# Performance work log

Hardware: AMD Instinct MI355X
Metric: run time of the kernel (lower is better)

## Reference

```python
import jax, jax.numpy as jnp
import numpy as np


def setup_inputs() -> dict:
    key = jax.random.key(0)
    k1, k2 = jax.random.split(key)
    B, H, S, D = 2, 16, 2048, 64
    scores = jax.random.normal(k1, (B, H, S, S), dtype=jnp.float32)
    v = jax.random.normal(k2, (B, H, S, D), dtype=jnp.float32)
    return {"scores": scores, "v": v}


def reference(scores, v):
    # softmax over last dim of [B,H,S,S], then contract with V [B,H,S,D]
    prob = jax.nn.softmax(scores, axis=-1)
    return jnp.einsum('bhqk,bhkd->bhqd', prob, v)
```

## Files before the change

### kernel.cpp

```cpp
#include <hip/hip_runtime.h>
#include <hip/hip_bf16.h>

#define NBH     32
#define SEQ     2048
#define DIM     64
#define QBLK    64
#define KBLK    64
#define NCHUNK  (SEQ / KBLK)
#define PSTRIDE 72

typedef __attribute__((ext_vector_type(4))) float f32x4;
typedef __attribute__((ext_vector_type(8))) short bf16x8;

__device__ __forceinline__ unsigned short bfbits(float f) {
    return __builtin_bit_cast(unsigned short, __float2bfloat16(f));
}

__global__ __launch_bounds__(256)
void vprep_kernel(const float* __restrict__ v, unsigned short* __restrict__ wsv)
{
    const int blk = blockIdx.x;
    const int bh  = blk >> 5, t = blk & 31;
    const float* vp = v + ((size_t)bh * SEQ + t * KBLK) * DIM;
    unsigned short* op = wsv + (size_t)blk * 4096;

    for (int fl = threadIdx.x; fl < 512; fl += 256) {
        const int ks = fl >> 8, dt = (fl >> 6) & 3, lane = fl & 63;
        const int g = lane >> 4, c = lane & 15;
        const float* sp = vp + (ks * 32 + g * 8) * DIM + dt * 16 + c;
        bf16x8 frag;
#pragma unroll
        for (int j = 0; j < 8; ++j)
            frag[j] = (short)bfbits(sp[j * DIM]);
        *reinterpret_cast<bf16x8*>(op + fl * 8) = frag;
    }
}

__global__ __launch_bounds__(256, 4)
void softmaxv_kernel(const float* __restrict__ scores,
                     const unsigned short* __restrict__ vfrags,
                     float* __restrict__ out)
{
    __shared__ unsigned short p_lds[2][QBLK * PSTRIDE];
    __shared__ float l_lds[QBLK];

    const int tid  = threadIdx.x;
    const int w    = tid >> 6;
    const int lane = tid & 63;
    const int g    = lane >> 4;
    const int c    = lane & 15;

    const int bid = blockIdx.x;
    const int bh  = bid >> 5;
    const int qb  = bid & 31;
    const int q0  = qb * QBLK;

    const float* sp = scores + ((size_t)bh * SEQ + q0 + w * 16 + g) * SEQ + c * 4;
    const unsigned short* vb = vfrags + (size_t)bh * 32 * 4096 + lane * 8;

    float lsum[4] = {0.f, 0.f, 0.f, 0.f};
    f32x4 acc[4];
#pragma unroll
    for (int dt = 0; dt < 4; ++dt) acc[dt] = (f32x4)0.0f;

#define LOADS(dst, t)                                                          \
    {                                                                          \
        _Pragma("unroll")                                                      \
        for (int i = 0; i < 4; ++i)                                            \
            dst[i] = *reinterpret_cast<const f32x4*>(                          \
                sp + (size_t)(i * 4) * SEQ + (t) * KBLK);                      \
    }

    auto proc = [&](const f32x4 (&sreg)[4], int t, unsigned short* pbuf) {
        const unsigned short* vp = vb + t * 4096;
        bf16x8 vf[2][4];
#pragma unroll
        for (int ks = 0; ks < 2; ++ks)
#pragma unroll
            for (int dt = 0; dt < 4; ++dt)
                vf[ks][dt] = *reinterpret_cast<const bf16x8*>(vp + (ks * 4 + dt) * 512);

#pragma unroll
        for (int i = 0; i < 4; ++i) {
            f32x4 s4 = sreg[i];
            float p0 = __expf(s4[0]);
            float p1 = __expf(s4[1]);
            float p2 = __expf(s4[2]);
            float p3 = __expf(s4[3]);
            lsum[i] += (p0 + p1) + (p2 + p3);
            unsigned lo = (unsigned)bfbits(p0) | ((unsigned)bfbits(p1) << 16);
            unsigned hi = (unsigned)bfbits(p2) | ((unsigned)bfbits(p3) << 16);
            const int row = w * 16 + i * 4 + g;
            *reinterpret_cast<uint2*>(&pbuf[row * PSTRIDE + c * 4]) = make_uint2(lo, hi);
        }

        __syncthreads();

#pragma unroll
        for (int ks = 0; ks < 2; ++ks) {
            const bf16x8 a = *reinterpret_cast<const bf16x8*>(
                &pbuf[(w * 16 + c) * PSTRIDE + ks * 32 + g * 8]);
#pragma unroll
            for (int dt = 0; dt < 4; ++dt)
                acc[dt] = __builtin_amdgcn_mfma_f32_16x16x32_bf16(
                    a, vf[ks][dt], acc[dt], 0, 0, 0);
        }
    };

    f32x4 sA[4], sB[4];
    LOADS(sA, 0)
    for (int tt = 0; tt < NCHUNK / 2; ++tt) {
        const int t0 = 2 * tt, t1 = 2 * tt + 1;
        LOADS(sB, t1)
        proc(sA, t0, p_lds[0]);
        if (t1 + 1 < NCHUNK) LOADS(sA, t1 + 1)
        proc(sB, t1, p_lds[1]);
    }
#undef LOADS

#pragma unroll
    for (int i = 0; i < 4; ++i) {
        float l = lsum[i];
        l += __shfl_xor(l, 1);
        l += __shfl_xor(l, 2);
        l += __shfl_xor(l, 4);
        l += __shfl_xor(l, 8);
        if (c == 0) l_lds[w * 16 + i * 4 + g] = l;
    }
    __syncthreads();

    float* op = out + ((size_t)bh * SEQ + q0 + w * 16) * DIM;
    float rl[4];
#pragma unroll
    for (int r = 0; r < 4; ++r)
        rl[r] = 1.0f / l_lds[w * 16 + g * 4 + r];
#pragma unroll
    for (int dt = 0; dt < 4; ++dt)
#pragma unroll
        for (int r = 0; r < 4; ++r)
            op[(g * 4 + r) * DIM + dt * 16 + c] = acc[dt][r] * rl[r];
}

extern "C" void kernel_launch(void* const* d_in, const int* in_sizes, int n_in,
                              void* d_out, int out_size, void* d_ws, size_t ws_size,
                              hipStream_t stream)
{
    const float* scores = (const float*)d_in[0];
    const float* v      = (const float*)d_in[1];
    float* out          = (float*)d_out;
    unsigned short* wsv = (unsigned short*)d_ws;

    vprep_kernel<<<dim3(NBH * NCHUNK), dim3(256), 0, stream>>>(v, wsv);
    softmaxv_kernel<<<dim3(NBH * (SEQ / QBLK)), dim3(256), 0, stream>>>(scores, wsv, out);
}
```

Before: 138.3 us.

## Load scores directly in MFMA A-fragment layout, dropping LDS staging and barriers

Each lane now reads its score row segments in the exact layout the bf16 MFMA A operand expects, so exponentials are packed into register fragments directly. This removes the LDS write/read round trip of the probability tile and the per-chunk __syncthreads. Row sums are reduced with cross-lane shuffles instead of LDS. The global load pattern changes from 16 lanes covering one contiguous 64-float row segment to each lane reading two 32-byte pieces of its own row, which may reduce coalescing on a memory-bound stream.

After: 150.3 us. 1.09x slower.

```diff
diff --git a/kernel.cpp b/kernel.cpp
--- a/kernel.cpp
+++ b/kernel.cpp
@@ -7,7 +7,6 @@
 #define QBLK    64
 #define KBLK    64
 #define NCHUNK  (SEQ / KBLK)
-#define PSTRIDE 72
 
 typedef __attribute__((ext_vector_type(4))) float f32x4;
 typedef __attribute__((ext_vector_type(8))) short bf16x8;
@@ -41,9 +40,6 @@
                      const unsigned short* __restrict__ vfrags,
                      float* __restrict__ out)
 {
-    __shared__ unsigned short p_lds[2][QBLK * PSTRIDE];
-    __shared__ float l_lds[QBLK];
-
     const int tid  = threadIdx.x;
     const int w    = tid >> 6;
     const int lane = tid & 63;
@@ -55,90 +51,88 @@
     const int qb  = bid & 31;
     const int q0  = qb * QBLK;
 
-    const float* sp = scores + ((size_t)bh * SEQ + q0 + w * 16 + g) * SEQ + c * 4;
-    const unsigned short* vb = vfrags + (size_t)bh * 32 * 4096 + lane * 8;
+    const float* sp = scores + ((size_t)bh * SEQ + q0 + w * 16 + c) * SEQ + g * 8;
+    const unsigned short* vb = vfrags + (size_t)bh * NCHUNK * 4096 + lane * 8;
 
-    float lsum[4] = {0.f, 0.f, 0.f, 0.f};
     f32x4 acc[4];
 #pragma unroll
     for (int dt = 0; dt < 4; ++dt) acc[dt] = (f32x4)0.0f;
+    float lsum[4] = {0.f, 0.f, 0.f, 0.f};
 
-#define LOADS(dst, t)                                                          \
+#define SLOADS(dst, t)                                                         \
     {                                                                          \
-        _Pragma("unroll")                                                      \
-        for (int i = 0; i < 4; ++i)                                            \
-            dst[i] = *reinterpret_cast<const f32x4*>(                          \
-                sp + (size_t)(i * 4) * SEQ + (t) * KBLK);                      \
+        dst[0] = *reinterpret_cast<const f32x4*>(sp + (t) * 64 + 0);           \
+        dst[1] = *reinterpret_cast<const f32x4*>(sp + (t) * 64 + 4);           \
+        dst[2] = *reinterpret_cast<const f32x4*>(sp + (t) * 64 + 32);          \
+        dst[3] = *reinterpret_cast<const f32x4*>(sp + (t) * 64 + 36);          \
     }
 
-    auto proc = [&](const f32x4 (&sreg)[4], int t, unsigned short* pbuf) {
-        const unsigned short* vp = vb + t * 4096;
-        bf16x8 vf[2][4];
+#define VLOAD(vf, t)                                                           \
+    {                                                                          \
+        const unsigned short* vp = vb + (t) * 4096;                            \
+        _Pragma("unroll")                                                      \
+        for (int ks = 0; ks < 2; ++ks)                                         \
+            _Pragma("unroll")                                                  \
+            for (int dt = 0; dt < 4; ++dt)                                     \
+                vf[ks][dt] = *reinterpret_cast<const bf16x8*>(                 \
+                    vp + (ks * 4 + dt) * 512);                                 \
+    }
+
+    auto compute = [&](const f32x4 (&sreg)[4], const bf16x8 (&vf)[2][4]) {
+        bf16x8 pfrag[2];
+#pragma unroll
+        for (int ks = 0; ks < 2; ++ks) {
+            const f32x4 a = sreg[ks * 2], b = sreg[ks * 2 + 1];
+            float e0 = __expf(a[0]), e1 = __expf(a[1]);
+            float e2 = __expf(a[2]), e3 = __expf(a[3]);
+            float e4 = __expf(b[0]), e5 = __expf(b[1]);
+            float e6 = __expf(b[2]), e7 = __expf(b[3]);
+            lsum[ks * 2]     += (e0 + e1) + (e2 + e3);
+            lsum[ks * 2 + 1] += (e4 + e5) + (e6 + e7);
+            bf16x8 p;
+            p[0] = (short)bfbits(e0); p[1] = (short)bfbits(e1);
+            p[2] = (short)bfbits(e2); p[3] = (short)bfbits(e3);
+            p[4] = (short)bfbits(e4); p[5] = (short)bfbits(e5);
+            p[6] = (short)bfbits(e6); p[7] = (short)bfbits(e7);
+            pfrag[ks] = p;
+        }
 #pragma unroll
         for (int ks = 0; ks < 2; ++ks)
 #pragma unroll
             for (int dt = 0; dt < 4; ++dt)
-                vf[ks][dt] = *reinterpret_cast<const bf16x8*>(vp + (ks * 4 + dt) * 512);
-
-#pragma unroll
-        for (int i = 0; i < 4; ++i) {
-            f32x4 s4 = sreg[i];
-            float p0 = __expf(s4[0]);
-            float p1 = __expf(s4[1]);
-            float p2 = __expf(s4[2]);
-            float p3 = __expf(s4[3]);
-            lsum[i] += (p0 + p1) + (p2 + p3);
-            unsigned lo = (unsigned)bfbits(p0) | ((unsigned)bfbits(p1) << 16);
-            unsigned hi = (unsigned)bfbits(p2) | ((unsigned)bfbits(p3) << 16);
-            const int row = w * 16 + i * 4 + g;
-            *reinterpret_cast<uint2*>(&pbuf[row * PSTRIDE + c * 4]) = make_uint2(lo, hi);
-        }
-
-        __syncthreads();
-
-#pragma unroll
-        for (int ks = 0; ks < 2; ++ks) {
-            const bf16x8 a = *reinterpret_cast<const bf16x8*>(
-                &pbuf[(w * 16 + c) * PSTRIDE + ks * 32 + g * 8]);
-#pragma unroll
-            for (int dt = 0; dt < 4; ++dt)
                 acc[dt] = __builtin_amdgcn_mfma_f32_16x16x32_bf16(
-                    a, vf[ks][dt], acc[dt], 0, 0, 0);
-        }
+                    pfrag[ks], vf[ks][dt], acc[dt], 0, 0, 0);
     };
 
     f32x4 sA[4], sB[4];
-    LOADS(sA, 0)
-    for (int tt = 0; tt < NCHUNK / 2; ++tt) {
-        const int t0 = 2 * tt, t1 = 2 * tt + 1;
-        LOADS(sB, t1)
-        proc(sA, t0, p_lds[0]);
-        if (t1 + 1 < NCHUNK) LOADS(sA, t1 + 1)
-        proc(sB, t1, p_lds[1]);
+    SLOADS(sA, 0)
+    for (int t = 0; t < NCHUNK; t += 2) {
+        bf16x8 vfA[2][4];
+        VLOAD(vfA, t)
+        SLOADS(sB, t + 1)
+        compute(sA, vfA);
+        bf16x8 vfB[2][4];
+        VLOAD(vfB, t + 1)
+        if (t + 2 < NCHUNK) SLOADS(sA, t + 2)
+        compute(sB, vfB);
     }
-#undef LOADS
+#undef SLOADS
+#undef VLOAD
 
+    float l = (lsum[0] + lsum[1]) + (lsum[2] + lsum[3]);
+    l += __shfl_xor(l, 16);
+    l += __shfl_xor(l, 32);
+    float rinv[4];
 #pragma unroll
-    for (int i = 0; i < 4; ++i) {
-        float l = lsum[i];
-        l += __shfl_xor(l, 1);
-        l += __shfl_xor(l, 2);
-        l += __shfl_xor(l, 4);
-        l += __shfl_xor(l, 8);
-        if (c == 0) l_lds[w * 16 + i * 4 + g] = l;
-    }
-    __syncthreads();
+    for (int r = 0; r < 4; ++r)
+        rinv[r] = 1.0f / __shfl(l, g * 4 + r);
 
     float* op = out + ((size_t)bh * SEQ + q0 + w * 16) * DIM;
-    float rl[4];
-#pragma unroll
-    for (int r = 0; r < 4; ++r)
-        rl[r] = 1.0f / l_lds[w * 16 + g * 4 + r];
 #pragma unroll
     for (int dt = 0; dt < 4; ++dt)
 #pragma unroll
         for (int r = 0; r < 4; ++r)
-            op[(g * 4 + r) * DIM + dt * 16 + c] = acc[dt][r] * rl[r];
+            op[(g * 4 + r) * DIM + dt * 16 + c] = acc[dt][r] * rinv[r];
 }
 
 extern "C" void kernel_launch(void* const* d_in, const int* in_sizes, int n_in,
```

## Use per-wave LDS P buffers to drop block barriers and prefetch V fragments

Applied to the files above, without the earlier changes.

Each wave now writes and reads its own 16-row slice of the P tile in private LDS buffers, so the __syncthreads between the P store and the MFMA A-fragment load is removed. V fragment loads are hoisted out of the per-chunk body and software-pipelined alongside the score loads, one chunk ahead. Without a wave barrier, correctness relies on in-wave ordering of the LDS writes and reads. Holding the prefetched V fragments in registers raises register pressure, which could hurt occupancy at the 4-blocks-per-SIMD launch bound.

Measured after the change: 200.2 us. +44.8%, slower.

```diff
diff --git a/kernel.cpp b/kernel.cpp
--- a/kernel.cpp
+++ b/kernel.cpp
@@ -7,7 +7,7 @@
 #define QBLK    64
 #define KBLK    64
 #define NCHUNK  (SEQ / KBLK)
-#define PSTRIDE 72
+#define PSTR    72
 
 typedef __attribute__((ext_vector_type(4))) float f32x4;
 typedef __attribute__((ext_vector_type(8))) short bf16x8;
@@ -41,7 +41,7 @@
                      const unsigned short* __restrict__ vfrags,
                      float* __restrict__ out)
 {
-    __shared__ unsigned short p_lds[2][QBLK * PSTRIDE];
+    __shared__ unsigned short p_lds[4][2][16 * PSTR];
     __shared__ float l_lds[QBLK];
 
     const int tid  = threadIdx.x;
@@ -56,14 +56,17 @@
     const int q0  = qb * QBLK;
 
     const float* sp = scores + ((size_t)bh * SEQ + q0 + w * 16 + g) * SEQ + c * 4;
-    const unsigned short* vb = vfrags + (size_t)bh * 32 * 4096 + lane * 8;
+    const unsigned short* vb = vfrags + (size_t)bh * NCHUNK * 4096 + lane * 8;
+
+    unsigned short* pb0 = &p_lds[w][0][0];
+    unsigned short* pb1 = &p_lds[w][1][0];
 
     float lsum[4] = {0.f, 0.f, 0.f, 0.f};
     f32x4 acc[4];
 #pragma unroll
     for (int dt = 0; dt < 4; ++dt) acc[dt] = (f32x4)0.0f;
 
-#define LOADS(dst, t)                                                          \
+#define SLOADS(dst, t)                                                         \
     {                                                                          \
         _Pragma("unroll")                                                      \
         for (int i = 0; i < 4; ++i)                                            \
@@ -71,15 +74,19 @@
                 sp + (size_t)(i * 4) * SEQ + (t) * KBLK);                      \
     }
 
-    auto proc = [&](const f32x4 (&sreg)[4], int t, unsigned short* pbuf) {
-        const unsigned short* vp = vb + t * 4096;
-        bf16x8 vf[2][4];
-#pragma unroll
-        for (int ks = 0; ks < 2; ++ks)
-#pragma unroll
-            for (int dt = 0; dt < 4; ++dt)
-                vf[ks][dt] = *reinterpret_cast<const bf16x8*>(vp + (ks * 4 + dt) * 512);
+#define VLOAD(vf, t)                                                           \
+    {                                                                          \
+        const unsigned short* vp = vb + (t) * 4096;                            \
+        _Pragma("unroll")                                                      \
+        for (int ks = 0; ks < 2; ++ks)                                         \
+            _Pragma("unroll")                                                  \
+            for (int dt = 0; dt < 4; ++dt)                                     \
+                vf[ks][dt] = *reinterpret_cast<const bf16x8*>(                 \
+                    vp + (ks * 4 + dt) * 512);                                 \
+    }
 
+    auto proc = [&](const f32x4 (&sreg)[4], const bf16x8 (&vf)[2][4],
+                    unsigned short* pbuf) {
 #pragma unroll
         for (int i = 0; i < 4; ++i) {
             f32x4 s4 = sreg[i];
@@ -90,16 +97,13 @@
             lsum[i] += (p0 + p1) + (p2 + p3);
             unsigned lo = (unsigned)bfbits(p0) | ((unsigned)bfbits(p1) << 16);
             unsigned hi = (unsigned)bfbits(p2) | ((unsigned)bfbits(p3) << 16);
-            const int row = w * 16 + i * 4 + g;
-            *reinterpret_cast<uint2*>(&pbuf[row * PSTRIDE + c * 4]) = make_uint2(lo, hi);
+            *reinterpret_cast<uint2*>(&pbuf[(i * 4 + g) * PSTR + c * 4]) =
+                make_uint2(lo, hi);
         }
-
-        __syncthreads();
-
 #pragma unroll
         for (int ks = 0; ks < 2; ++ks) {
             const bf16x8 a = *reinterpret_cast<const bf16x8*>(
-                &pbuf[(w * 16 + c) * PSTRIDE + ks * 32 + g * 8]);
+                &pbuf[c * PSTR + ks * 32 + g * 8]);
 #pragma unroll
             for (int dt = 0; dt < 4; ++dt)
                 acc[dt] = __builtin_amdgcn_mfma_f32_16x16x32_bf16(
@@ -108,15 +112,21 @@
     };
 
     f32x4 sA[4], sB[4];
-    LOADS(sA, 0)
-    for (int tt = 0; tt < NCHUNK / 2; ++tt) {
-        const int t0 = 2 * tt, t1 = 2 * tt + 1;
-        LOADS(sB, t1)
-        proc(sA, t0, p_lds[0]);
-        if (t1 + 1 < NCHUNK) LOADS(sA, t1 + 1)
-        proc(sB, t1, p_lds[1]);
+    bf16x8 vfA[2][4], vfB[2][4];
+    SLOADS(sA, 0)
+    VLOAD(vfA, 0)
+    for (int t = 0; t < NCHUNK; t += 2) {
+        VLOAD(vfB, t + 1)
+        SLOADS(sB, t + 1)
+        proc(sA, vfA, pb0);
+        if (t + 2 < NCHUNK) {
+            VLOAD(vfA, t + 2)
+            SLOADS(sA, t + 2)
+        }
+        proc(sB, vfB, pb1);
     }
-#undef LOADS
+#undef SLOADS
+#undef VLOAD
 
 #pragma unroll
     for (int i = 0; i < 4; ++i) {
```
